# Optimization experiments

Hardware: AMD Instinct MI355X
Metric: run time of the kernel (lower is better)

Reference implementation:

```python
import jax, jax.numpy as jnp
import numpy as np

EMBED_DIM = 1024
NUM_HEADS = 16
HEAD_DIM = EMBED_DIM // NUM_HEADS
FF_DIM = 4096
B, T, S = 2, 2048, 2048
LN_EPS = 1e-5


def setup_inputs() -> dict:
    key = jax.random.key(0)
    ks = jax.random.split(key, 20)
    sd = 1.0 / np.sqrt(EMBED_DIM)
    d = {
        'x': jax.random.normal(ks[0], (B, T, EMBED_DIM), jnp.float32),
        'encoder_outputs': jax.random.normal(ks[1], (B, S, EMBED_DIM), jnp.float32),
        'tgt_mask': jnp.tril(jnp.ones((T, T), bool))[None, None],  # [1,1,T,T] causal
    }
    # weights stored [in, out] so y = x @ W + b
    names = ['sa_wq', 'sa_wk', 'sa_wv', 'sa_wo', 'ca_wq', 'ca_wk', 'ca_wv', 'ca_wo']
    for i, n in enumerate(names):
        d[n] = jax.random.normal(ks[2 + i], (EMBED_DIM, EMBED_DIM), jnp.float32) * sd
        d[n.replace('w', 'b')] = jnp.zeros((EMBED_DIM,), jnp.float32)
    d['ff_w1'] = jax.random.normal(ks[10], (EMBED_DIM, FF_DIM), jnp.float32) * sd
    d['ff_b1'] = jnp.zeros((FF_DIM,), jnp.float32)
    d['ff_w2'] = jax.random.normal(ks[11], (FF_DIM, EMBED_DIM), jnp.float32) * (1.0 / np.sqrt(FF_DIM))
    d['ff_b2'] = jnp.zeros((EMBED_DIM,), jnp.float32)
    for i in (1, 2, 3):
        d[f'ln{i}_g'] = jnp.ones((EMBED_DIM,), jnp.float32)
        d[f'ln{i}_b'] = jnp.zeros((EMBED_DIM,), jnp.float32)
    return d


def _layernorm(x, g, b):
    mu = jnp.mean(x, -1, keepdims=True)
    var = jnp.mean(jnp.square(x - mu), -1, keepdims=True)
    return (x - mu) * jax.lax.rsqrt(var + LN_EPS) * g + b


def _mha(q_in, k_in, v_in, wq, bq, wk, bk, wv, bv, wo, bo, mask=None):
    Bq, Tq, C = q_in.shape
    Tk = k_in.shape[1]
    Q = (q_in @ wq + bq).reshape(Bq, Tq, NUM_HEADS, HEAD_DIM)
    K = (k_in @ wk + bk).reshape(Bq, Tk, NUM_HEADS, HEAD_DIM)
    V = (v_in @ wv + bv).reshape(Bq, Tk, NUM_HEADS, HEAD_DIM)
    scores = jnp.einsum('bqhd,bkhd->bhqk', Q, K) / np.sqrt(HEAD_DIM)
    if mask is not None:
        scores = jnp.where(mask, scores, -jnp.inf)
    attn = jax.nn.softmax(scores, axis=-1)
    out = jnp.einsum('bhqk,bkhd->bqhd', attn, V).reshape(Bq, Tq, C)
    return out @ wo + bo


def reference(x, encoder_outputs, tgt_mask,
              sa_wq, sa_bq, sa_wk, sa_bk, sa_wv, sa_bv, sa_wo, sa_bo,
              ca_wq, ca_bq, ca_wk, ca_bk, ca_wv, ca_bv, ca_wo, ca_bo,
              ff_w1, ff_b1, ff_w2, ff_b2,
              ln1_g, ln1_b, ln2_g, ln2_b, ln3_g, ln3_b):
    h = _layernorm(x, ln1_g, ln1_b)
    x = x + _mha(h, h, h, sa_wq, sa_bq, sa_wk, sa_bk, sa_wv, sa_bv, sa_wo, sa_bo, tgt_mask)
    h = _layernorm(x, ln2_g, ln2_b)
    x = x + _mha(h, encoder_outputs, encoder_outputs,
                 ca_wq, ca_bq, ca_wk, ca_bk, ca_wv, ca_bv, ca_wo, ca_bo, None)
    h = _layernorm(x, ln3_g, ln3_b)
    ff = jax.nn.relu(h @ ff_w1 + ff_b1) @ ff_w2 + ff_b2
    return x + ff
```

## Files before the change

kernel.cpp:

```cpp
#include <hip/hip_runtime.h>
#include <stdint.h>


typedef __bf16 bf16x8 __attribute__((ext_vector_type(8)));
typedef float  f32x4  __attribute__((ext_vector_type(4)));

#define T_SEQ 2048
#define NROWS 4096
#define QSCALE 0.18033688011112042f

__device__ __forceinline__ unsigned short f2bf(float f) {
  union { float f; unsigned int u; } v; v.f = f;
  unsigned int u = v.u;
  return (unsigned short)((u + 0x7FFFu + ((u >> 16) & 1u)) >> 16);
}
__device__ __forceinline__ float bf2f(unsigned short h) {
  union { unsigned int u; float f; } v; v.u = ((unsigned int)h) << 16;
  return v.f;
}
__device__ __forceinline__ unsigned int pk2(float a, float b) {
  return (unsigned int)f2bf(a) | ((unsigned int)f2bf(b) << 16);
}
__device__ __forceinline__ unsigned int pk2t(float a, float b) {
  union { float f; unsigned int u; } ua, ub;
  ua.f = a; ub.f = b;
  return __builtin_amdgcn_perm(ub.u, ua.u, 0x07060302u);
}
union U4 { unsigned int u[4]; bf16x8 v; };

__global__ void probe_dtype_kernel(const unsigned short* __restrict__ p,
                                   int* __restrict__ flag) {
  __shared__ int cnt;
  if (threadIdx.x == 0) cnt = 0;
  __syncthreads();
  int bad = 0;
  for (int i = threadIdx.x; i < 4096; i += 256) {
    unsigned short u = p[i];
    int e = (u >> 7) & 0xFF;
    if (u != 0 && (e < 100 || e > 140)) bad++;
  }
  atomicAdd(&cnt, bad);
  __syncthreads();
  if (threadIdx.x == 0) *flag = (cnt < 512) ? 1 : 0;
}

struct WTbl {
  const void* src[10];
  int K[10], N[10], start[10];
  unsigned int dstoff[10];
};
__global__ void wtrans_fused_kernel(WTbl tbl, unsigned short* __restrict__ wsbase,
                                    const int* __restrict__ flag) {
  __shared__ unsigned short tile[32][33];
  const int lb = blockIdx.x;
  int wi = 0;
#pragma unroll
  for (int i = 1; i < 10; i++) wi = (lb >= tbl.start[i]) ? i : wi;
  const int local = lb - tbl.start[wi];
  const int Nw = tbl.N[wi], Kw = tbl.K[wi];
  const int bx = local & ((Nw >> 5) - 1);
  const int by = local / (Nw >> 5);
  const void* W = tbl.src[wi];
  unsigned short* Wt = wsbase + tbl.dstoff[wi];
  const int n0 = bx * 32, k0 = by * 32;
  const int c = threadIdx.x & 31, r0 = threadIdx.x >> 5;
  const bool isbf = (*flag != 0);
  for (int r = r0; r < 32; r += 8) {
    unsigned short v;
    if (isbf) v = ((const unsigned short*)W)[(size_t)(k0 + r) * Nw + n0 + c];
    else      v = f2bf(((const float*)W)[(size_t)(k0 + r) * Nw + n0 + c]);
    tile[r][c] = v;
  }
  __syncthreads();
  for (int r = r0; r < 32; r += 8)
    Wt[(size_t)(n0 + r) * Kw + k0 + c] = tile[c][r];
}

struct PTbl { const void* p[19]; };
__global__ void param_cvt_kernel(PTbl tbl, float* __restrict__ out,
                                 const int* __restrict__ flag) {
  const int blk = blockIdx.x;
  const int off = (blk >= 8 && blk < 12) ? (blk - 8) * 1024 : 0;
  const void* src = tbl.p[blk];
  const int i = threadIdx.x * 4;
  float4 o;
  if (*flag) {
    const unsigned short* u = (const unsigned short*)src + off;
    ushort4 q = *(const ushort4*)&u[i];
    o.x = bf2f(q.x); o.y = bf2f(q.y); o.z = bf2f(q.z); o.w = bf2f(q.w);
  } else {
    o = *(const float4*)&((const float*)src)[off + i];
  }
  *(float4*)&out[blk * 1024 + i] = o;
}

__global__ void cvt_to_bf16_kernel(const void* __restrict__ in,
                                   unsigned short* __restrict__ out,
                                   int n, const int* __restrict__ flag) {
  int i = (blockIdx.x * 256 + threadIdx.x) * 8;
  if (i >= n) return;
  if (*flag) {
    *(int4*)&out[i] = *(const int4*)&((const unsigned short*)in)[i];
  } else {
    const float* f = (const float*)in;
    float4 a = *(const float4*)&f[i];
    float4 c = *(const float4*)&f[i + 4];
    ushort4 o1, o2;
    o1.x = f2bf(a.x); o1.y = f2bf(a.y); o1.z = f2bf(a.z); o1.w = f2bf(a.w);
    o2.x = f2bf(c.x); o2.y = f2bf(c.y); o2.z = f2bf(c.z); o2.w = f2bf(c.w);
    *(ushort4*)&out[i] = o1;
    *(ushort4*)&out[i + 4] = o2;
  }
}

__global__ void cvt_to_f32_kernel(const void* __restrict__ in,
                                  float* __restrict__ out,
                                  int n, const int* __restrict__ flag) {
  int i = (blockIdx.x * 256 + threadIdx.x) * 4;
  if (i >= n) return;
  if (*flag) {
    const unsigned short* u = (const unsigned short*)in;
    ushort4 q = *(const ushort4*)&u[i];
    float4 o;
    o.x = bf2f(q.x); o.y = bf2f(q.y); o.z = bf2f(q.z); o.w = bf2f(q.w);
    *(float4*)&out[i] = o;
  } else {
    *(float4*)&out[i] = *(const float4*)&((const float*)in)[i];
  }
}

__global__ __launch_bounds__(256) void ln_kernel(
    const float* __restrict__ x, const float* __restrict__ g,
    const float* __restrict__ b, unsigned short* __restrict__ out) {
  const int row = blockIdx.x;
  const int t = threadIdx.x;
  const size_t base = (size_t)row * 1024;
  float4 v = *(const float4*)&x[base + t * 4];
  float s1 = v.x + v.y + v.z + v.w;
  float s2 = v.x * v.x + v.y * v.y + v.z * v.z + v.w * v.w;
#pragma unroll
  for (int d = 1; d < 64; d <<= 1) {
    s1 += __shfl_xor(s1, d, 64);
    s2 += __shfl_xor(s2, d, 64);
  }
  __shared__ float a1[4], a2[4];
  if ((t & 63) == 0) { a1[t >> 6] = s1; a2[t >> 6] = s2; }
  __syncthreads();
  s1 = a1[0] + a1[1] + a1[2] + a1[3];
  s2 = a2[0] + a2[1] + a2[2] + a2[3];
  const float mean = s1 * (1.0f / 1024.0f);
  const float var = s2 * (1.0f / 1024.0f) - mean * mean;
  const float rstd = rsqrtf(fmaxf(var, 0.0f) + 1e-5f);
  float4 gv = *(const float4*)&g[t * 4];
  float4 bv = *(const float4*)&b[t * 4];
  ushort4 o;
  o.x = f2bf((v.x - mean) * rstd * gv.x + bv.x);
  o.y = f2bf((v.y - mean) * rstd * gv.y + bv.y);
  o.z = f2bf((v.z - mean) * rstd * gv.z + bv.z);
  o.w = f2bf((v.w - mean) * rstd * gv.w + bv.w);
  *(ushort4*)&out[base + t * 4] = o;
}

template <int BM, int BN, int BK, int RELU, int RESID, int OUTM, int BIASROW,
          int SCALEMODE>
__global__ __launch_bounds__(256, 2) void gemm_kernel(
    const unsigned short* __restrict__ A, const unsigned short* __restrict__ Bt,
    const float* __restrict__ bias, const float* __restrict__ resid,
    void* __restrict__ outp, int M, int N, int K,
    const int* __restrict__ flag) {
  static_assert(BK == 64, "swizzle assumes 8 chunks/row");
  constexpr int WX = (BN == 64) ? 1 : 2;
  constexpr int WY = 4 / WX;
  constexpr int WM = BM / WY, WN = BN / WX;
  constexpr int MI = WM / 16, NJ = WN / 16;
  constexpr int ACALLS = BM * BK / 2048;
  constexpr int BCALLS = BN * BK / 2048;
  constexpr int RPC = 2048 / BK;
  __shared__ unsigned short lsA[BM * BK];
  __shared__ unsigned short lsB[BN * BK];
  const int t = threadIdx.x;
  const int wave = t >> 6, lane = t & 63;
  const int ml = lane & 15, quad = lane >> 4;
  const int cx = ml & 7;
  const int wm = (wave / WX) * WM, wn = (wave % WX) * WN;

  const int nx = gridDim.x, ny = gridDim.y;
  const int lin = (int)blockIdx.y * nx + (int)blockIdx.x;
  const int per = 8 * nx;
  const int y0 = (lin / per) * 8;
  const int gsz = (ny - y0 < 8) ? (ny - y0) : 8;
  const int by = y0 + (lin % gsz);
  const int bx = (lin % per) / gsz;
  const size_t m0 = (size_t)by * BM;
  const size_t n0 = (size_t)bx * BN;

  f32x4 acc[MI][NJ];
  const f32x4 fz = {0.f, 0.f, 0.f, 0.f};
#pragma unroll
  for (int i = 0; i < MI; i++)
#pragma unroll
    for (int j = 0; j < NJ; j++) acc[i][j] = fz;

  const int rowL = t >> 3;
  const int colL = (((t & 7) ^ ((t >> 3) & 7)) * 8);
  const unsigned short* gA = A + (m0 + rowL) * (size_t)K + colL;
  const unsigned short* gB = Bt + (n0 + rowL) * (size_t)K + colL;

  for (int k0 = 0; k0 < K; k0 += BK) {
    __syncthreads();
#pragma unroll
    for (int c = 0; c < ACALLS; c++)
      __builtin_amdgcn_global_load_lds(
          (const __attribute__((address_space(1))) void*)(gA + (size_t)(c * RPC) * K + k0),
          (__attribute__((address_space(3))) void*)&lsA[c * 2048 + wave * 512], 16, 0, 0);
#pragma unroll
    for (int c = 0; c < BCALLS; c++)
      __builtin_amdgcn_global_load_lds(
          (const __attribute__((address_space(1))) void*)(gB + (size_t)(c * RPC) * K + k0),
          (__attribute__((address_space(3))) void*)&lsB[c * 2048 + wave * 512], 16, 0, 0);
    __syncthreads();
#pragma unroll
    for (int h = 0; h < BK / 32; h++) {
      bf16x8 af[MI], bfv[NJ];
#pragma unroll
      for (int i = 0; i < MI; i++)
        af[i] = *(const bf16x8*)
            &lsA[(wm + i * 16 + ml) * BK + (((h * 4 + quad) ^ cx) * 8)];
#pragma unroll
      for (int j = 0; j < NJ; j++)
        bfv[j] = *(const bf16x8*)
            &lsB[(wn + j * 16 + ml) * BK + (((h * 4 + quad) ^ cx) * 8)];
#pragma unroll
      for (int i = 0; i < MI; i++)
#pragma unroll
        for (int j = 0; j < NJ; j++)
          acc[i][j] = __builtin_amdgcn_mfma_f32_16x16x32_bf16(af[i], bfv[j],
                                                              acc[i][j], 0, 0, 0);
    }
  }

  const bool obf = (OUTM == 1) || (OUTM == 2 && *flag != 0);
#pragma unroll
  for (int j = 0; j < NJ; j++) {
    const size_t cg = n0 + wn + j * 16 + ml;
    const float bcol = BIASROW ? 0.0f : bias[cg];
    const float sc = (SCALEMODE == 0) ? 1.0f
                   : (SCALEMODE == 1) ? QSCALE
                                      : (cg < 1024 ? QSCALE : 1.0f);
#pragma unroll
    for (int i = 0; i < MI; i++) {
#pragma unroll
      for (int r = 0; r < 4; r++) {
        const size_t rg = m0 + wm + i * 16 + quad * 4 + r;
        const float bval = BIASROW ? bias[rg] : bcol;
        float v = (acc[i][j][r] + bval) * sc;
        if (RELU) v = fmaxf(v, 0.0f);
        if (RESID) v += resid[rg * N + cg];
        if (obf) ((unsigned short*)outp)[rg * N + cg] = f2bf(v);
        else     ((float*)outp)[rg * N + cg] = v;
      }
    }
  }
}

template <int CAUSAL>
__global__ __launch_bounds__(256, 4) void attn_kernel(
    const unsigned short* __restrict__ Q, const unsigned short* __restrict__ K,
    const unsigned short* __restrict__ VT, unsigned short* __restrict__ O,
    int qstride, int kstride) {
  __shared__ unsigned short Ks[4096];
  __shared__ unsigned short Vs[4096];
  __shared__ unsigned short Qs[4608];
  const int t = threadIdx.x;
  const int wave = t >> 6, lane = t & 63;
  const int ml = lane & 15, quad = lane >> 4;
  const int cx = ml & 7;
  const int bh = blockIdx.y, b = bh >> 4, h = bh & 15;
  const int qb = CAUSAL ? ((int)gridDim.x - 1 - (int)blockIdx.x) : (int)blockIdx.x;
  const int q0 = qb * 64;
  const int lr = lane >> 3;
  const int scol = (((lane & 7) ^ lr) * 8);

  {
    const unsigned short* g0 =
        Q + ((size_t)(b * T_SEQ + q0 + wave * 16 + lr)) * qstride + h * 64 + scol;
    __builtin_amdgcn_global_load_lds(
        (const __attribute__((address_space(1))) void*)g0,
        (__attribute__((address_space(3))) void*)&Qs[wave * 2 * 512], 16, 0, 0);
    const unsigned short* g1 = g0 + (size_t)8 * qstride;
    __builtin_amdgcn_global_load_lds(
        (const __attribute__((address_space(1))) void*)g1,
        (__attribute__((address_space(3))) void*)&Qs[(wave * 2 + 1) * 512], 16, 0, 0);
  }

  int sp_[2];
#pragma unroll
  for (int i = 0; i < 2; i++) {
    int p = (wave * 2 + i) * 8 + lr;
    sp_[i] = ((p & 16) << 1) | ((p & 12) << 1) | ((p & 32) >> 3) | (p & 3);
  }
  const unsigned short* Kb_ = K + ((size_t)b * T_SEQ) * kstride + h * 64 + scol;
  const unsigned short* Vb_ = VT + ((size_t)h * 64) * 4096 + (size_t)b * T_SEQ + scol;

  __syncthreads();
  const bf16x8 aq0 = *(const bf16x8*)&Qs[(wave * 16 + ml) * 64 + ((quad ^ cx) * 8)];
  const bf16x8 aq1 = *(const bf16x8*)&Qs[(wave * 16 + ml) * 64 + (((quad + 4) ^ cx) * 8)];

  f32x4 acc[4];
  const f32x4 fz = {0.f, 0.f, 0.f, 0.f};
#pragma unroll
  for (int n = 0; n < 4; n++) acc[n] = fz;
  float m_i = -3.0e38f, l_i = 0.0f;
  const int q_glob = q0 + wave * 16 + ml;
  const int nkb = CAUSAL ? (qb + 1) : (T_SEQ / 64);

  for (int kb = 0; kb < nkb; kb++) {
    __syncthreads();
#pragma unroll
    for (int i = 0; i < 2; i++) {
      const int c = wave * 2 + i;
      const unsigned short* kg = Kb_ + ((size_t)(kb * 64 + sp_[i])) * kstride;
      __builtin_amdgcn_global_load_lds(
          (const __attribute__((address_space(1))) void*)kg,
          (__attribute__((address_space(3))) void*)&Ks[c * 512], 16, 0, 0);
      const unsigned short* vg = Vb_ + (size_t)(c * 8 + lr) * 4096 + kb * 64;
      __builtin_amdgcn_global_load_lds(
          (const __attribute__((address_space(1))) void*)vg,
          (__attribute__((address_space(3))) void*)&Vs[c * 512], 16, 0, 0);
    }
    __syncthreads();

    f32x4 s[4];
#pragma unroll
    for (int nt = 0; nt < 4; nt++) {
      bf16x8 k0 = *(const bf16x8*)&Ks[(nt * 16 + ml) * 64 + ((quad ^ cx) * 8)];
      bf16x8 k1 = *(const bf16x8*)&Ks[(nt * 16 + ml) * 64 + (((quad + 4) ^ cx) * 8)];
      f32x4 a = fz;
      a = __builtin_amdgcn_mfma_f32_16x16x32_bf16(k0, aq0, a, 0, 0, 0);
      a = __builtin_amdgcn_mfma_f32_16x16x32_bf16(k1, aq1, a, 0, 0, 0);
      s[nt] = a;
    }
    if (CAUSAL && kb == nkb - 1) {
#pragma unroll
      for (int nt = 0; nt < 4; nt++)
#pragma unroll
        for (int r = 0; r < 4; r++) {
          int key = kb * 64 + ((nt & 1) << 5) + (quad << 3) + ((nt >> 1) << 2) + r;
          if (key > q_glob) s[nt][r] = -3.0e38f;
        }
    }
    float tm = -3.0e38f;
#pragma unroll
    for (int nt = 0; nt < 4; nt++)
#pragma unroll
      for (int r = 0; r < 4; r++) tm = fmaxf(tm, s[nt][r]);
    tm = fmaxf(tm, __shfl_xor(tm, 16));
    tm = fmaxf(tm, __shfl_xor(tm, 32));
    const float m_new = fmaxf(m_i, tm);
    const float alpha = exp2f(m_i - m_new);
    float p[4][4];
    float rs = 0.f;
#pragma unroll
    for (int nt = 0; nt < 4; nt++)
#pragma unroll
      for (int r = 0; r < 4; r++) {
        p[nt][r] = exp2f(s[nt][r] - m_new);
        rs += p[nt][r];
      }
    rs += __shfl_xor(rs, 16);
    rs += __shfl_xor(rs, 32);
    l_i = l_i * alpha + rs;
    m_i = m_new;
#pragma unroll
    for (int n = 0; n < 4; n++)
#pragma unroll
      for (int r = 0; r < 4; r++) acc[n][r] *= alpha;

    U4 P0, P1;
    P0.u[0] = pk2t(p[0][0], p[0][1]); P0.u[1] = pk2t(p[0][2], p[0][3]);
    P0.u[2] = pk2t(p[2][0], p[2][1]); P0.u[3] = pk2t(p[2][2], p[2][3]);
    P1.u[0] = pk2t(p[1][0], p[1][1]); P1.u[1] = pk2t(p[1][2], p[1][3]);
    P1.u[2] = pk2t(p[3][0], p[3][1]); P1.u[3] = pk2t(p[3][2], p[3][3]);

#pragma unroll
    for (int n = 0; n < 4; n++) {
      bf16x8 v0 = *(const bf16x8*)&Vs[(n * 16 + ml) * 64 + ((quad ^ cx) * 8)];
      bf16x8 v1 = *(const bf16x8*)&Vs[(n * 16 + ml) * 64 + (((quad + 4) ^ cx) * 8)];
      acc[n] = __builtin_amdgcn_mfma_f32_16x16x32_bf16(v0, P0.v, acc[n], 0, 0, 0);
      acc[n] = __builtin_amdgcn_mfma_f32_16x16x32_bf16(v1, P1.v, acc[n], 0, 0, 0);
    }
  }

  const float inv = 1.0f / l_i;
#pragma unroll
  for (int n = 0; n < 4; n++)
#pragma unroll
    for (int rp = 0; rp < 2; rp++) {
      unsigned int u = pk2(acc[n][2 * rp] * inv, acc[n][2 * rp + 1] * inv);
      *(unsigned int*)&Qs[(wave * 16 + ml) * 72 + n * 16 + quad * 4 + 2 * rp] = u;
    }
  __syncthreads();
  {
    const int q = t >> 2, d0 = (t & 3) * 16;
    unsigned short* og = O + ((size_t)(b * T_SEQ + q0 + q)) * 1024 + h * 64 + d0;
    *(int4*)og = *(const int4*)&Qs[q * 72 + d0];
    *(int4*)(og + 8) = *(const int4*)&Qs[q * 72 + d0 + 8];
  }
}

extern "C" void kernel_launch(void* const* d_in, const int* in_sizes, int n_in,
                              void* d_out, int out_size, void* d_ws,
                              size_t ws_size, hipStream_t stream) {
  (void)in_sizes; (void)n_in; (void)out_size; (void)ws_size;
  const size_t MEG = 1048576;
  unsigned short* ws16 = (unsigned short*)d_ws;
  char* wsb = (char*)d_ws;

  unsigned short* wt[10];
  for (int i = 0; i < 8; i++) wt[i] = ws16 + (size_t)i * MEG;
  wt[8] = ws16 + 8 * MEG;
  wt[9] = ws16 + 12 * MEG;
  unsigned short* encB  = ws16 + 16 * MEG;
  unsigned short* hbuf  = ws16 + 20 * MEG;
  unsigned short* QKb   = ws16 + 24 * MEG;
  unsigned short* Qb    = ws16 + 32 * MEG;
  unsigned short* Kb    = ws16 + 36 * MEG;
  unsigned short* Vb    = ws16 + 40 * MEG;
  unsigned short* attnb = ws16 + 44 * MEG;
  unsigned short* ffh   = ws16 + 24 * MEG;
  float* xf32 = (float*)(wsb + 96 * MEG);
  float* pbuf = (float*)(wsb + 112 * MEG);
  int* flag   = (int*)(wsb + 113 * MEG);

  probe_dtype_kernel<<<1, 256, 0, stream>>>((const unsigned short*)d_in[0], flag);

  {
    WTbl tb;
    const int widx[10] = {3, 5, 7, 9, 11, 13, 15, 17, 19, 21};
    int st = 0;
    for (int i = 0; i < 10; i++) {
      tb.src[i] = d_in[widx[i]];
      tb.K[i] = (i == 9) ? 4096 : 1024;
      tb.N[i] = (i == 8) ? 4096 : 1024;
      tb.start[i] = st;
      st += (tb.K[i] / 32) * (tb.N[i] / 32);
      tb.dstoff[i] = (unsigned int)((i < 8) ? i * MEG : (i == 8 ? 8 * MEG : 12 * MEG));
    }
    wtrans_fused_kernel<<<16384, 256, 0, stream>>>(tb, ws16, flag);
  }

  cvt_to_f32_kernel<<<4096, 256, 0, stream>>>(d_in[0], xf32, 4194304, flag);
  cvt_to_bf16_kernel<<<2048, 256, 0, stream>>>(d_in[1], encB, 4194304, flag);

  {
    PTbl pt;
    const int pidx[19] = {4, 6, 8, 10, 12, 14, 16, 18,
                          20, 20, 20, 20, 22, 23, 24, 25, 26, 27, 28};
    for (int i = 0; i < 19; i++) pt.p[i] = d_in[pidx[i]];
    param_cvt_kernel<<<19, 256, 0, stream>>>(pt, pbuf, flag);
  }
  float* bqk_sa = pbuf;
  float* bv_sa  = pbuf + 2048;
  float* bo_sa  = pbuf + 3072;
  float* bq_ca  = pbuf + 4096;
  float* bk_ca  = pbuf + 5120;
  float* bv_ca  = pbuf + 6144;
  float* bo_ca  = pbuf + 7168;
  float* ff_b1p = pbuf + 8192;
  float* ff_b2p = pbuf + 12288;
  float* ln1g = pbuf + 13312; float* ln1b = pbuf + 14336;
  float* ln2g = pbuf + 15360; float* ln2b = pbuf + 16384;
  float* ln3g = pbuf + 17408; float* ln3b = pbuf + 18432;

  dim3 gQK(16, 32);
  dim3 gP(16, 32);
  dim3 gVT(64, 8);
  dim3 gFF1(32, 32);
  dim3 gFF2(8, 64);
  dim3 gAttn(32, 32);

  ln_kernel<<<4096, 256, 0, stream>>>(xf32, ln1g, ln1b, hbuf);
  gemm_kernel<128, 128, 64, 0, 0, 1, 0, 2><<<gQK, 256, 0, stream>>>(
      hbuf, wt[0], bqk_sa, nullptr, QKb, NROWS, 2048, 1024, nullptr);
  gemm_kernel<128, 64, 64, 0, 0, 1, 1, 0><<<gVT, 256, 0, stream>>>(
      wt[2], hbuf, bv_sa, nullptr, Vb, 1024, 4096, 1024, nullptr);
  attn_kernel<1><<<gAttn, 256, 0, stream>>>(QKb, QKb + 1024, Vb, attnb, 2048, 2048);
  gemm_kernel<128, 64, 64, 0, 1, 0, 0, 0><<<gP, 256, 0, stream>>>(
      attnb, wt[3], bo_sa, xf32, xf32, NROWS, 1024, 1024, nullptr);

  ln_kernel<<<4096, 256, 0, stream>>>(xf32, ln2g, ln2b, hbuf);
  gemm_kernel<128, 64, 64, 0, 0, 1, 0, 1><<<gP, 256, 0, stream>>>(
      hbuf, wt[4], bq_ca, nullptr, Qb, NROWS, 1024, 1024, nullptr);
  gemm_kernel<128, 64, 64, 0, 0, 1, 0, 0><<<gP, 256, 0, stream>>>(
      encB, wt[5], bk_ca, nullptr, Kb, NROWS, 1024, 1024, nullptr);
  gemm_kernel<128, 64, 64, 0, 0, 1, 1, 0><<<gVT, 256, 0, stream>>>(
      wt[6], encB, bv_ca, nullptr, Vb, 1024, 4096, 1024, nullptr);
  attn_kernel<0><<<gAttn, 256, 0, stream>>>(Qb, Kb, Vb, attnb, 1024, 1024);
  gemm_kernel<128, 64, 64, 0, 1, 0, 0, 0><<<gP, 256, 0, stream>>>(
      attnb, wt[7], bo_ca, xf32, xf32, NROWS, 1024, 1024, nullptr);

  ln_kernel<<<4096, 256, 0, stream>>>(xf32, ln3g, ln3b, hbuf);
  gemm_kernel<128, 128, 64, 1, 0, 1, 0, 0><<<gFF1, 256, 0, stream>>>(
      hbuf, wt[8], ff_b1p, nullptr, ffh, NROWS, 4096, 1024, nullptr);
  gemm_kernel<64, 128, 64, 0, 1, 2, 0, 0><<<gFF2, 256, 0, stream>>>(
      ffh, wt[9], ff_b2p, xf32, d_out, NROWS, 1024, 4096, flag);
}
```

Before: 610.9 us.

## Merge projection GEMMs into multi-segment launches and streamline attention softmax

Adds a grouped GEMM kernel that runs several independent projection GEMMs (self-attn QK+V, cross-attn Q, K, V) in one launch with grouped block rasterization. This cuts launch count and lets small GEMMs fill the GPU together. The QK projection now uses 128x64 tiles instead of 128x128. In attention, the online-softmax rescale is skipped when no row max changes, the hardware exp2 intrinsic is used, the row-sum shuffle reduction is deferred to the end, and K/V pointers are advanced incrementally. The cost is runtime segment dispatch and a branch per key block.

```diff
diff --git a/kernel.cpp b/kernel.cpp
--- a/kernel.cpp
+++ b/kernel.cpp
@@ -25,6 +25,9 @@
   union { float f; unsigned int u; } ua, ub;
   ua.f = a; ub.f = b;
   return __builtin_amdgcn_perm(ub.u, ua.u, 0x07060302u);
+}
+__device__ __forceinline__ float fexp2(float x) {
+  return __builtin_amdgcn_exp2f(x);
 }
 union U4 { unsigned int u[4]; bf16x8 v; };
 
@@ -263,6 +266,103 @@
   }
 }
 
+struct GSeg {
+  const unsigned short* A; const unsigned short* B;
+  const float* bias; unsigned short* out;
+  int N, K, start, gxlog2, mode;
+};
+template <int NSEG>
+__global__ __launch_bounds__(256, 4) void gemm_multi_kernel(GSeg s0, GSeg s1,
+                                                            GSeg s2) {
+  constexpr int BM = 128, BN = 64, BK = 64;
+  constexpr int WM = 32, WN = 64;
+  constexpr int MI = 2, NJ = 4;
+  __shared__ unsigned short lsA[BM * BK];
+  __shared__ unsigned short lsB[BN * BK];
+  const int blk = (int)blockIdx.x;
+  GSeg sg = s0;
+  if (NSEG > 1 && blk >= s1.start) sg = s1;
+  if (NSEG > 2 && blk >= s2.start) sg = s2;
+  const int t = threadIdx.x;
+  const int wave = t >> 6, lane = t & 63;
+  const int ml = lane & 15, quad = lane >> 4;
+  const int cx = ml & 7;
+  const int wm = wave * WM, wn = 0;
+  const int N = sg.N, K = sg.K;
+
+  const int lin = blk - sg.start;
+  const int per = 8 << sg.gxlog2;
+  const int y0 = (lin / per) * 8;
+  const int by = y0 + (lin & 7);
+  const int bx = (lin & (per - 1)) >> 3;
+  const size_t m0 = (size_t)by * BM;
+  const size_t n0 = (size_t)bx * BN;
+
+  f32x4 acc[MI][NJ];
+  const f32x4 fz = {0.f, 0.f, 0.f, 0.f};
+#pragma unroll
+  for (int i = 0; i < MI; i++)
+#pragma unroll
+    for (int j = 0; j < NJ; j++) acc[i][j] = fz;
+
+  const int rowL = t >> 3;
+  const int colL = (((t & 7) ^ ((t >> 3) & 7)) * 8);
+  const unsigned short* gA = sg.A + (m0 + rowL) * (size_t)K + colL;
+  const unsigned short* gB = sg.B + (n0 + rowL) * (size_t)K + colL;
+
+  for (int k0 = 0; k0 < K; k0 += BK) {
+    __syncthreads();
+#pragma unroll
+    for (int c = 0; c < 4; c++)
+      __builtin_amdgcn_global_load_lds(
+          (const __attribute__((address_space(1))) void*)(gA + (size_t)(c * 32) * K + k0),
+          (__attribute__((address_space(3))) void*)&lsA[c * 2048 + wave * 512], 16, 0, 0);
+#pragma unroll
+    for (int c = 0; c < 2; c++)
+      __builtin_amdgcn_global_load_lds(
+          (const __attribute__((address_space(1))) void*)(gB + (size_t)(c * 32) * K + k0),
+          (__attribute__((address_space(3))) void*)&lsB[c * 2048 + wave * 512], 16, 0, 0);
+    __syncthreads();
+#pragma unroll
+    for (int h = 0; h < BK / 32; h++) {
+      bf16x8 af[MI], bfv[NJ];
+#pragma unroll
+      for (int i = 0; i < MI; i++)
+        af[i] = *(const bf16x8*)
+            &lsA[(wm + i * 16 + ml) * BK + (((h * 4 + quad) ^ cx) * 8)];
+#pragma unroll
+      for (int j = 0; j < NJ; j++)
+        bfv[j] = *(const bf16x8*)
+            &lsB[(wn + j * 16 + ml) * BK + (((h * 4 + quad) ^ cx) * 8)];
+#pragma unroll
+      for (int i = 0; i < MI; i++)
+#pragma unroll
+        for (int j = 0; j < NJ; j++)
+          acc[i][j] = __builtin_amdgcn_mfma_f32_16x16x32_bf16(af[i], bfv[j],
+                                                              acc[i][j], 0, 0, 0);
+    }
+  }
+
+  const int mode = sg.mode;
+#pragma unroll
+  for (int j = 0; j < NJ; j++) {
+    const size_t cg = n0 + wn + j * 16 + ml;
+    const float bcol = (mode & 1) ? 0.0f : sg.bias[cg];
+    const float sc = (mode & 2) ? QSCALE
+                   : ((mode & 4) && cg < 1024) ? QSCALE : 1.0f;
+#pragma unroll
+    for (int i = 0; i < MI; i++) {
+#pragma unroll
+      for (int r = 0; r < 4; r++) {
+        const size_t rg = m0 + wm + i * 16 + quad * 4 + r;
+        const float bval = (mode & 1) ? sg.bias[rg] : bcol;
+        float v = (acc[i][j][r] + bval) * sc;
+        sg.out[rg * N + cg] = f2bf(v);
+      }
+    }
+  }
+}
+
 template <int CAUSAL>
 __global__ __launch_bounds__(256, 4) void attn_kernel(
     const unsigned short* __restrict__ Q, const unsigned short* __restrict__ K,
@@ -299,8 +399,13 @@
     int p = (wave * 2 + i) * 8 + lr;
     sp_[i] = ((p & 16) << 1) | ((p & 12) << 1) | ((p & 32) >> 3) | (p & 3);
   }
-  const unsigned short* Kb_ = K + ((size_t)b * T_SEQ) * kstride + h * 64 + scol;
-  const unsigned short* Vb_ = VT + ((size_t)h * 64) * 4096 + (size_t)b * T_SEQ + scol;
+  const unsigned short* kg0 =
+      K + ((size_t)b * T_SEQ + sp_[0]) * kstride + h * 64 + scol;
+  const unsigned short* kg1 =
+      K + ((size_t)b * T_SEQ + sp_[1]) * kstride + h * 64 + scol;
+  const unsigned short* vg0 =
+      VT + ((size_t)(h * 64 + wave * 16 + lr)) * 4096 + (size_t)b * T_SEQ + scol;
+  const unsigned short* vg1 = vg0 + (size_t)8 * 4096;
 
   __syncthreads();
   const bf16x8 aq0 = *(const bf16x8*)&Qs[(wave * 16 + ml) * 64 + ((quad ^ cx) * 8)];
@@ -310,24 +415,26 @@
   const f32x4 fz = {0.f, 0.f, 0.f, 0.f};
 #pragma unroll
   for (int n = 0; n < 4; n++) acc[n] = fz;
-  float m_i = -3.0e38f, l_i = 0.0f;
+  float m_i = -3.0e38f, l_part = 0.0f;
   const int q_glob = q0 + wave * 16 + ml;
   const int nkb = CAUSAL ? (qb + 1) : (T_SEQ / 64);
+  const size_t kinc = (size_t)64 * kstride;
 
   for (int kb = 0; kb < nkb; kb++) {
     __syncthreads();
-#pragma unroll
-    for (int i = 0; i < 2; i++) {
-      const int c = wave * 2 + i;
-      const unsigned short* kg = Kb_ + ((size_t)(kb * 64 + sp_[i])) * kstride;
-      __builtin_amdgcn_global_load_lds(
-          (const __attribute__((address_space(1))) void*)kg,
-          (__attribute__((address_space(3))) void*)&Ks[c * 512], 16, 0, 0);
-      const unsigned short* vg = Vb_ + (size_t)(c * 8 + lr) * 4096 + kb * 64;
-      __builtin_amdgcn_global_load_lds(
-          (const __attribute__((address_space(1))) void*)vg,
-          (__attribute__((address_space(3))) void*)&Vs[c * 512], 16, 0, 0);
-    }
+    __builtin_amdgcn_global_load_lds(
+        (const __attribute__((address_space(1))) void*)kg0,
+        (__attribute__((address_space(3))) void*)&Ks[(wave * 2) * 512], 16, 0, 0);
+    __builtin_amdgcn_global_load_lds(
+        (const __attribute__((address_space(1))) void*)kg1,
+        (__attribute__((address_space(3))) void*)&Ks[(wave * 2 + 1) * 512], 16, 0, 0);
+    __builtin_amdgcn_global_load_lds(
+        (const __attribute__((address_space(1))) void*)vg0,
+        (__attribute__((address_space(3))) void*)&Vs[(wave * 2) * 512], 16, 0, 0);
+    __builtin_amdgcn_global_load_lds(
+        (const __attribute__((address_space(1))) void*)vg1,
+        (__attribute__((address_space(3))) void*)&Vs[(wave * 2 + 1) * 512], 16, 0, 0);
+    kg0 += kinc; kg1 += kinc; vg0 += 64; vg1 += 64;
     __syncthreads();
 
     f32x4 s[4];
@@ -356,25 +463,26 @@
       for (int r = 0; r < 4; r++) tm = fmaxf(tm, s[nt][r]);
     tm = fmaxf(tm, __shfl_xor(tm, 16));
     tm = fmaxf(tm, __shfl_xor(tm, 32));
-    const float m_new = fmaxf(m_i, tm);
-    const float alpha = exp2f(m_i - m_new);
+    if (__any(tm > m_i)) {
+      const float m_new = fmaxf(m_i, tm);
+      const float alpha = fexp2(m_i - m_new);
+      l_part *= alpha;
+#pragma unroll
+      for (int n = 0; n < 4; n++)
+#pragma unroll
+        for (int r = 0; r < 4; r++) acc[n][r] *= alpha;
+      m_i = m_new;
+    }
     float p[4][4];
     float rs = 0.f;
 #pragma unroll
     for (int nt = 0; nt < 4; nt++)
 #pragma unroll
       for (int r = 0; r < 4; r++) {
-        p[nt][r] = exp2f(s[nt][r] - m_new);
+        p[nt][r] = fexp2(s[nt][r] - m_i);
         rs += p[nt][r];
       }
-    rs += __shfl_xor(rs, 16);
-    rs += __shfl_xor(rs, 32);
-    l_i = l_i * alpha + rs;
-    m_i = m_new;
-#pragma unroll
-    for (int n = 0; n < 4; n++)
-#pragma unroll
-      for (int r = 0; r < 4; r++) acc[n][r] *= alpha;
+    l_part += rs;
 
     U4 P0, P1;
     P0.u[0] = pk2t(p[0][0], p[0][1]); P0.u[1] = pk2t(p[0][2], p[0][3]);
@@ -390,6 +498,10 @@
       acc[n] = __builtin_amdgcn_mfma_f32_16x16x32_bf16(v1, P1.v, acc[n], 0, 0, 0);
     }
   }
+
+  float l_i = l_part;
+  l_i += __shfl_xor(l_i, 16);
+  l_i += __shfl_xor(l_i, 32);
 
   const float inv = 1.0f / l_i;
 #pragma unroll
@@ -472,29 +584,28 @@
   float* ln2g = pbuf + 15360; float* ln2b = pbuf + 16384;
   float* ln3g = pbuf + 17408; float* ln3b = pbuf + 18432;
 
-  dim3 gQK(16, 32);
   dim3 gP(16, 32);
-  dim3 gVT(64, 8);
   dim3 gFF1(32, 32);
   dim3 gFF2(8, 64);
   dim3 gAttn(32, 32);
 
   ln_kernel<<<4096, 256, 0, stream>>>(xf32, ln1g, ln1b, hbuf);
-  gemm_kernel<128, 128, 64, 0, 0, 1, 0, 2><<<gQK, 256, 0, stream>>>(
-      hbuf, wt[0], bqk_sa, nullptr, QKb, NROWS, 2048, 1024, nullptr);
-  gemm_kernel<128, 64, 64, 0, 0, 1, 1, 0><<<gVT, 256, 0, stream>>>(
-      wt[2], hbuf, bv_sa, nullptr, Vb, 1024, 4096, 1024, nullptr);
+  {
+    GSeg sQK = {hbuf, wt[0], bqk_sa, QKb, 2048, 1024, 0, 5, 4};
+    GSeg sVT = {wt[2], hbuf, bv_sa, Vb, 4096, 1024, 1024, 6, 1};
+    gemm_multi_kernel<2><<<1536, 256, 0, stream>>>(sQK, sVT, sVT);
+  }
   attn_kernel<1><<<gAttn, 256, 0, stream>>>(QKb, QKb + 1024, Vb, attnb, 2048, 2048);
   gemm_kernel<128, 64, 64, 0, 1, 0, 0, 0><<<gP, 256, 0, stream>>>(
       attnb, wt[3], bo_sa, xf32, xf32, NROWS, 1024, 1024, nullptr);
 
   ln_kernel<<<4096, 256, 0, stream>>>(xf32, ln2g, ln2b, hbuf);
-  gemm_kernel<128, 64, 64, 0, 0, 1, 0, 1><<<gP, 256, 0, stream>>>(
-      hbuf, wt[4], bq_ca, nullptr, Qb, NROWS, 1024, 1024, nullptr);
-  gemm_kernel<128, 64, 64, 0, 0, 1, 0, 0><<<gP, 256, 0, stream>>>(
-      encB, wt[5], bk_ca, nullptr, Kb, NROWS, 1024, 1024, nullptr);
-  gemm_kernel<128, 64, 64, 0, 0, 1, 1, 0><<<gVT, 256, 0, stream>>>(
-      wt[6], encB, bv_ca, nullptr, Vb, 1024, 4096, 1024, nullptr);
+  {
+    GSeg sQ = {hbuf, wt[4], bq_ca, Qb, 1024, 1024, 0, 4, 2};
+    GSeg sK = {encB, wt[5], bk_ca, Kb, 1024, 1024, 512, 4, 0};
+    GSeg sV = {wt[6], encB, bv_ca, Vb, 4096, 1024, 1024, 6, 1};
+    gemm_multi_kernel<3><<<1536, 256, 0, stream>>>(sQ, sK, sV);
+  }
   attn_kernel<0><<<gAttn, 256, 0, stream>>>(Qb, Kb, Vb, attnb, 1024, 1024);
   gemm_kernel<128, 64, 64, 0, 1, 0, 0, 0><<<gP, 256, 0, stream>>>(
       attnb, wt[7], bo_ca, xf32, xf32, NROWS, 1024, 1024, nullptr);
```

Result: faster. 558.2 us (-8.6%).
